# Kernel tuning notes

Measured on AMD Instinct MI355X. Metric: run time of the kernel, lower is better.

The kernel has to match this reference:

```python
import jax, jax.numpy as jnp
import numpy as np

IN_DIM = 256
HIDDEN = 64


def setup_inputs() -> dict:
    key = jax.random.key(0)
    k1, k2, k3, k4, k5, k6 = jax.random.split(key, 6)
    N, M, D, H = 2048, 2048, IN_DIM, HIDDEN
    # Kaiming-uniform-ish init scales (matching nn.Linear defaults loosely)
    lim1 = 1.0 / np.sqrt(2 * D)
    lim2 = 1.0 / np.sqrt(H)
    return {
        "ag_embed": jax.random.normal(k1, (N, D), dtype=jnp.float32),
        "ab_embed": jax.random.normal(k2, (M, D), dtype=jnp.float32),
        "W1": jax.random.uniform(k3, (2 * D, H), dtype=jnp.float32, minval=-lim1, maxval=lim1),
        "b1": jax.random.uniform(k4, (H,), dtype=jnp.float32, minval=-lim1, maxval=lim1),
        "W2": jax.random.uniform(k5, (H,), dtype=jnp.float32, minval=-lim2, maxval=lim2),
        "b2": jax.random.uniform(k6, (), dtype=jnp.float32, minval=-lim2, maxval=lim2),
    }


def reference(ag_embed, ab_embed, W1, b1, W2, b2):
    # Fused broadcast-concat + first linear:
    # cat([ag, ab]) @ W1 == ag @ W1[:D] + ab @ W1[D:]  (same math, no NxMx2D tensor)
    D = ag_embed.shape[1]
    ag_h = ag_embed @ W1[:D] + b1          # [N, H]
    ab_h = ab_embed @ W1[D:]               # [M, H]
    h = jax.nn.relu(ag_h[:, None, :] + ab_h[None, :, :])   # [N, M, H]
    logits = jnp.einsum("nmh,h->nm", h, W2) + b2            # [N, M]
    return jax.nn.sigmoid(logits)
```

## Files before the change

### kernel.cpp

```cpp
#include <hip/hip_runtime.h>
#include <hip/hip_bf16.h>

typedef float v2f __attribute__((ext_vector_type(2)));
typedef float v4f __attribute__((ext_vector_type(4)));

#define DD 256
#define HH 64

__global__ __launch_bounds__(256) void prep_kernel(
    const float* __restrict__ ag, const float* __restrict__ ab,
    const float* __restrict__ W1, const float* __restrict__ b1,
    float* __restrict__ U, float* __restrict__ V)
{
    __shared__ float a_tile[16 * DD];
    __shared__ float w_tile[DD * HH];

    const int t = threadIdx.x;
    const int b = blockIdx.x;
    const bool isV = (b >= 128);
    const float* __restrict__ A = isV ? ab : ag;
    const int row0 = (isV ? b - 128 : b) * 16;
    const float* __restrict__ W = W1 + (isV ? DD * HH : 0);

    {
        const v4f* As = (const v4f*)(A + row0 * DD);
        v4f* Ad = (v4f*)a_tile;
        #pragma unroll
        for (int i = 0; i < 4; ++i) Ad[t + i * 256] = As[t + i * 256];
        const v4f* Ws = (const v4f*)W;
        v4f* Wd = (v4f*)w_tile;
        #pragma unroll
        for (int i = 0; i < 16; ++i) Wd[t + i * 256] = Ws[t + i * 256];
    }
    __syncthreads();

    const int h = t & 63;
    const int g = t >> 6;
    float acc0 = 0.f, acc1 = 0.f, acc2 = 0.f, acc3 = 0.f;
    const float* __restrict__ ar = a_tile + (g * 4) * DD;
    #pragma unroll 8
    for (int k = 0; k < DD; ++k) {
        const float w = w_tile[k * HH + h];
        acc0 += ar[k]          * w;
        acc1 += ar[k + DD]     * w;
        acc2 += ar[k + 2 * DD] * w;
        acc3 += ar[k + 3 * DD] * w;
    }

    if (!isV) {
        const float bb = b1[h];
        float* Ur = U + (row0 + g * 4) * HH + h;
        Ur[0]      = acc0 + bb;
        Ur[HH]     = acc1 + bb;
        Ur[2 * HH] = acc2 + bb;
        Ur[3 * HH] = acc3 + bb;
    } else {
        __syncthreads();
        float* buf = a_tile;
        buf[(g * 4 + 0) * HH + h] = acc0;
        buf[(g * 4 + 1) * HH + h] = acc1;
        buf[(g * 4 + 2) * HH + h] = acc2;
        buf[(g * 4 + 3) * HH + h] = acc3;
        __syncthreads();
        const int hs = t >> 2, q = t & 3;
        v4f f;
        f.x = buf[(q * 4 + 0) * HH + hs];
        f.y = buf[(q * 4 + 1) * HH + hs];
        f.z = buf[(q * 4 + 2) * HH + hs];
        f.w = buf[(q * 4 + 3) * HH + hs];
        *(v4f*)(V + hs * 2048 + row0 + q * 4) = f;
    }
}

__global__ __launch_bounds__(256) void pair_kernel(
    const float* __restrict__ U, const float* __restrict__ V,
    const float* __restrict__ W2, const float* __restrict__ b2,
    float* __restrict__ out)
{
    __shared__ float u_lds[32 * HH];
    __shared__ float vt[HH * 128];
    __shared__ float w2_lds[HH];

    const int t = threadIdx.x;
    const int R = blockIdx.y * 32;
    const int C = blockIdx.x * 128;

    {
        const v4f* Us = (const v4f*)(U + R * HH);
        v4f* Ud = (v4f*)u_lds;
        Ud[t]       = Us[t];
        Ud[t + 256] = Us[t + 256];
        const float* Vb = V + C;
        v4f* Vd = (v4f*)vt;
        #pragma unroll
        for (int i = 0; i < 8; ++i) {
            const int flat = t + i * 256;
            const int hh = flat >> 5;
            const int cc = flat & 31;
            Vd[flat] = *(const v4f*)(Vb + hh * 2048 + cc * 4);
        }
        if (t < HH) w2_lds[t] = W2[t];
    }
    __syncthreads();

    const int lane = t & 63;
    const int wv = t >> 6;
    const int r0 = wv * 8;
    const int c0 = lane * 2;

    v2f acc[8];
    #pragma unroll
    for (int i = 0; i < 8; ++i) acc[i] = 0.0f;

    const v2f vzero = 0.0f;
    #pragma unroll 2
    for (int h0 = 0; h0 < HH; h0 += 4) {
        const v4f w4 = *(const v4f*)&w2_lds[h0];
        const v2f vf0 = *(const v2f*)&vt[(h0 + 0) * 128 + c0];
        const v2f vf1 = *(const v2f*)&vt[(h0 + 1) * 128 + c0];
        const v2f vf2 = *(const v2f*)&vt[(h0 + 2) * 128 + c0];
        const v2f vf3 = *(const v2f*)&vt[(h0 + 3) * 128 + c0];
        #pragma unroll
        for (int i = 0; i < 8; ++i) {
            const v4f uf = *(const v4f*)&u_lds[(r0 + i) * HH + h0];
            v2f t0 = vf0 + uf.x; t0 = __builtin_elementwise_max(t0, vzero); acc[i] += t0 * w4.x;
            v2f t1 = vf1 + uf.y; t1 = __builtin_elementwise_max(t1, vzero); acc[i] += t1 * w4.y;
            v2f t2 = vf2 + uf.z; t2 = __builtin_elementwise_max(t2, vzero); acc[i] += t2 * w4.z;
            v2f t3 = vf3 + uf.w; t3 = __builtin_elementwise_max(t3, vzero); acc[i] += t3 * w4.w;
        }
    }

    const float b2v = *b2;
    #pragma unroll
    for (int i = 0; i < 8; ++i) {
        const v2f x = acc[i] + b2v;
        float2 st;
        st.x = 1.0f / (1.0f + __expf(-x.x));
        st.y = 1.0f / (1.0f + __expf(-x.y));
        *(float2*)(out + (size_t)(R + r0 + i) * 2048 + C + c0) = st;
    }
}

extern "C" void kernel_launch(void* const* d_in, const int* in_sizes, int n_in,
                              void* d_out, int out_size, void* d_ws, size_t ws_size,
                              hipStream_t stream) {
    const float* ag = (const float*)d_in[0];
    const float* ab = (const float*)d_in[1];
    const float* W1 = (const float*)d_in[2];
    const float* b1 = (const float*)d_in[3];
    const float* W2 = (const float*)d_in[4];
    const float* b2 = (const float*)d_in[5];
    float* out = (float*)d_out;

    float* U = (float*)d_ws;
    float* V = U + 2048 * HH;

    prep_kernel<<<256, 256, 0, stream>>>(ag, ab, W1, b1, U, V);
    pair_kernel<<<dim3(16, 64), 256, 0, stream>>>(U, V, W2, b2, out);
}
```

Baseline: 97.95 us.

## Use packed fp16 with fdot2 in pair kernel and restructure prep kernel

The pairwise kernel now stores U and V as packed half2 and does the add, relu and W2 dot with packed fp16 math plus v_dot2 instructions, so each instruction handles twice as many elements. The column tile per block doubles and each thread produces four outputs. The prep kernel reads inputs straight from global memory instead of staging whole tiles in LDS, and writes fp16 outputs through a small padded buffer. Sigmoid uses a fast reciprocal. Half-precision intermediates lower accuracy and may exceed tolerance.

```diff
diff --git a/kernel.cpp b/kernel.cpp
--- a/kernel.cpp
+++ b/kernel.cpp
@@ -3,141 +3,179 @@
 
 typedef float v2f __attribute__((ext_vector_type(2)));
 typedef float v4f __attribute__((ext_vector_type(4)));
+typedef _Float16 h2v __attribute__((ext_vector_type(2)));
 
 #define DD 256
 #define HH 64
+#define H2 32
+
+#if __has_builtin(__builtin_amdgcn_fdot2)
+#define FDOT2(a, b, c) __builtin_amdgcn_fdot2((a), (b), (c), false)
+#else
+#define FDOT2(a, b, c) ((c) + (float)(a).x * (float)(b).x + (float)(a).y * (float)(b).y)
+#endif
+
+static __device__ __forceinline__ h2v as_h2(unsigned x) {
+    union { unsigned u; h2v h; } c; c.u = x; return c.h;
+}
+static __device__ __forceinline__ float fast_sigmoid(float x) {
+    return __builtin_amdgcn_rcpf(1.0f + __expf(-x));
+}
 
 __global__ __launch_bounds__(256) void prep_kernel(
     const float* __restrict__ ag, const float* __restrict__ ab,
     const float* __restrict__ W1, const float* __restrict__ b1,
-    float* __restrict__ U, float* __restrict__ V)
+    h2v* __restrict__ U, h2v* __restrict__ V)
 {
-    __shared__ float a_tile[16 * DD];
-    __shared__ float w_tile[DD * HH];
+    __shared__ float buf[16 * 66];
 
     const int t = threadIdx.x;
     const int b = blockIdx.x;
     const bool isV = (b >= 128);
     const float* __restrict__ A = isV ? ab : ag;
-    const int row0 = (isV ? b - 128 : b) * 16;
+    const int row0 = (b & 127) * 16;
     const float* __restrict__ W = W1 + (isV ? DD * HH : 0);
-
-    {
-        const v4f* As = (const v4f*)(A + row0 * DD);
-        v4f* Ad = (v4f*)a_tile;
-        #pragma unroll
-        for (int i = 0; i < 4; ++i) Ad[t + i * 256] = As[t + i * 256];
-        const v4f* Ws = (const v4f*)W;
-        v4f* Wd = (v4f*)w_tile;
-        #pragma unroll
-        for (int i = 0; i < 16; ++i) Wd[t + i * 256] = Ws[t + i * 256];
-    }
-    __syncthreads();
 
     const int h = t & 63;
     const int g = t >> 6;
+    const float* __restrict__ a0 = A + (row0 + g * 4) * DD;
+
     float acc0 = 0.f, acc1 = 0.f, acc2 = 0.f, acc3 = 0.f;
-    const float* __restrict__ ar = a_tile + (g * 4) * DD;
-    #pragma unroll 8
-    for (int k = 0; k < DD; ++k) {
-        const float w = w_tile[k * HH + h];
-        acc0 += ar[k]          * w;
-        acc1 += ar[k + DD]     * w;
-        acc2 += ar[k + 2 * DD] * w;
-        acc3 += ar[k + 3 * DD] * w;
+    #pragma unroll 2
+    for (int k = 0; k < DD; k += 4) {
+        const float w0 = W[(k + 0) * HH + h];
+        const float w1 = W[(k + 1) * HH + h];
+        const float w2_ = W[(k + 2) * HH + h];
+        const float w3 = W[(k + 3) * HH + h];
+        const v4f aa0 = *(const v4f*)(a0 + k);
+        const v4f aa1 = *(const v4f*)(a0 + DD + k);
+        const v4f aa2 = *(const v4f*)(a0 + 2 * DD + k);
+        const v4f aa3 = *(const v4f*)(a0 + 3 * DD + k);
+        acc0 = fmaf(aa0.x, w0, acc0); acc0 = fmaf(aa0.y, w1, acc0);
+        acc0 = fmaf(aa0.z, w2_, acc0); acc0 = fmaf(aa0.w, w3, acc0);
+        acc1 = fmaf(aa1.x, w0, acc1); acc1 = fmaf(aa1.y, w1, acc1);
+        acc1 = fmaf(aa1.z, w2_, acc1); acc1 = fmaf(aa1.w, w3, acc1);
+        acc2 = fmaf(aa2.x, w0, acc2); acc2 = fmaf(aa2.y, w1, acc2);
+        acc2 = fmaf(aa2.z, w2_, acc2); acc2 = fmaf(aa2.w, w3, acc2);
+        acc3 = fmaf(aa3.x, w0, acc3); acc3 = fmaf(aa3.y, w1, acc3);
+        acc3 = fmaf(aa3.z, w2_, acc3); acc3 = fmaf(aa3.w, w3, acc3);
     }
 
     if (!isV) {
         const float bb = b1[h];
-        float* Ur = U + (row0 + g * 4) * HH + h;
-        Ur[0]      = acc0 + bb;
-        Ur[HH]     = acc1 + bb;
-        Ur[2 * HH] = acc2 + bb;
-        Ur[3 * HH] = acc3 + bb;
-    } else {
-        __syncthreads();
-        float* buf = a_tile;
-        buf[(g * 4 + 0) * HH + h] = acc0;
-        buf[(g * 4 + 1) * HH + h] = acc1;
-        buf[(g * 4 + 2) * HH + h] = acc2;
-        buf[(g * 4 + 3) * HH + h] = acc3;
-        __syncthreads();
-        const int hs = t >> 2, q = t & 3;
-        v4f f;
-        f.x = buf[(q * 4 + 0) * HH + hs];
-        f.y = buf[(q * 4 + 1) * HH + hs];
-        f.z = buf[(q * 4 + 2) * HH + hs];
-        f.w = buf[(q * 4 + 3) * HH + hs];
-        *(v4f*)(V + hs * 2048 + row0 + q * 4) = f;
+        acc0 += bb; acc1 += bb; acc2 += bb; acc3 += bb;
+    }
+
+    buf[(g * 4 + 0) * 66 + h] = acc0;
+    buf[(g * 4 + 1) * 66 + h] = acc1;
+    buf[(g * 4 + 2) * 66 + h] = acc2;
+    buf[(g * 4 + 3) * 66 + h] = acc3;
+    __syncthreads();
+
+    #pragma unroll
+    for (int i = 0; i < 2; ++i) {
+        const int flat = t + i * 256;
+        if (!isV) {
+            const int r = flat >> 5, h2 = flat & 31;
+            h2v p;
+            p.x = (_Float16)buf[r * 66 + 2 * h2];
+            p.y = (_Float16)buf[r * 66 + 2 * h2 + 1];
+            U[(row0 + r) * H2 + h2] = p;
+        } else {
+            const int c = flat & 15, h2 = flat >> 4;
+            h2v p;
+            p.x = (_Float16)buf[c * 66 + 2 * h2];
+            p.y = (_Float16)buf[c * 66 + 2 * h2 + 1];
+            V[h2 * 2048 + row0 + c] = p;
+        }
     }
 }
 
-__global__ __launch_bounds__(256) void pair_kernel(
-    const float* __restrict__ U, const float* __restrict__ V,
+__global__ __launch_bounds__(256, 2) void pair_kernel(
+    const h2v* __restrict__ U, const h2v* __restrict__ V,
     const float* __restrict__ W2, const float* __restrict__ b2,
     float* __restrict__ out)
 {
-    __shared__ float u_lds[32 * HH];
-    __shared__ float vt[HH * 128];
-    __shared__ float w2_lds[HH];
+    __shared__ unsigned u_lds[32 * H2];
+    __shared__ unsigned vt[H2 * 256];
+    __shared__ h2v w2l[H2];
 
     const int t = threadIdx.x;
     const int R = blockIdx.y * 32;
-    const int C = blockIdx.x * 128;
+    const int C = blockIdx.x * 256;
 
     {
-        const v4f* Us = (const v4f*)(U + R * HH);
-        v4f* Ud = (v4f*)u_lds;
-        Ud[t]       = Us[t];
-        Ud[t + 256] = Us[t + 256];
-        const float* Vb = V + C;
-        v4f* Vd = (v4f*)vt;
+        const uint4* Us = (const uint4*)(U + R * H2);
+        ((uint4*)u_lds)[t] = Us[t];
+        const uint4* Vs = (const uint4*)V;
+        uint4* Vd = (uint4*)vt;
         #pragma unroll
         for (int i = 0; i < 8; ++i) {
             const int flat = t + i * 256;
-            const int hh = flat >> 5;
-            const int cc = flat & 31;
-            Vd[flat] = *(const v4f*)(Vb + hh * 2048 + cc * 4);
+            const int row = flat >> 6, c4 = flat & 63;
+            Vd[flat] = Vs[row * 512 + (C >> 2) + c4];
         }
-        if (t < HH) w2_lds[t] = W2[t];
+        if (t < H2) {
+            h2v p; p.x = (_Float16)W2[2 * t]; p.y = (_Float16)W2[2 * t + 1];
+            w2l[t] = p;
+        }
     }
     __syncthreads();
 
     const int lane = t & 63;
     const int wv = t >> 6;
     const int r0 = wv * 8;
-    const int c0 = lane * 2;
 
-    v2f acc[8];
+    float acc[8][4];
     #pragma unroll
-    for (int i = 0; i < 8; ++i) acc[i] = 0.0f;
+    for (int i = 0; i < 8; ++i)
+        #pragma unroll
+        for (int k = 0; k < 4; ++k) acc[i][k] = 0.0f;
 
-    const v2f vzero = 0.0f;
-    #pragma unroll 2
-    for (int h0 = 0; h0 < HH; h0 += 4) {
-        const v4f w4 = *(const v4f*)&w2_lds[h0];
-        const v2f vf0 = *(const v2f*)&vt[(h0 + 0) * 128 + c0];
-        const v2f vf1 = *(const v2f*)&vt[(h0 + 1) * 128 + c0];
-        const v2f vf2 = *(const v2f*)&vt[(h0 + 2) * 128 + c0];
-        const v2f vf3 = *(const v2f*)&vt[(h0 + 3) * 128 + c0];
+    const h2v zero = {(_Float16)0.0f, (_Float16)0.0f};
+    const uint4* ub = (const uint4*)u_lds;
+    const uint4* vb = (const uint4*)vt;
+
+    #pragma unroll
+    for (int hc = 0; hc < 8; ++hc) {
+        const uint4 wq = *((const uint4*)w2l + hc);
+        const h2v w0 = as_h2(wq.x), w1 = as_h2(wq.y), w2_ = as_h2(wq.z), w3 = as_h2(wq.w);
+
+        h2v vv[4][4];
+        #pragma unroll
+        for (int j = 0; j < 4; ++j) {
+            const uint4 q = vb[(hc * 4 + j) * 64 + lane];
+            vv[j][0] = as_h2(q.x); vv[j][1] = as_h2(q.y);
+            vv[j][2] = as_h2(q.z); vv[j][3] = as_h2(q.w);
+        }
+
         #pragma unroll
         for (int i = 0; i < 8; ++i) {
-            const v4f uf = *(const v4f*)&u_lds[(r0 + i) * HH + h0];
-            v2f t0 = vf0 + uf.x; t0 = __builtin_elementwise_max(t0, vzero); acc[i] += t0 * w4.x;
-            v2f t1 = vf1 + uf.y; t1 = __builtin_elementwise_max(t1, vzero); acc[i] += t1 * w4.y;
-            v2f t2 = vf2 + uf.z; t2 = __builtin_elementwise_max(t2, vzero); acc[i] += t2 * w4.z;
-            v2f t3 = vf3 + uf.w; t3 = __builtin_elementwise_max(t3, vzero); acc[i] += t3 * w4.w;
+            const uint4 uq = ub[(r0 + i) * 8 + hc];
+            const h2v u0 = as_h2(uq.x), u1 = as_h2(uq.y), u2 = as_h2(uq.z), u3 = as_h2(uq.w);
+            #pragma unroll
+            for (int k = 0; k < 4; ++k) {
+                h2v s0 = u0 + vv[0][k]; s0 = __builtin_elementwise_max(s0, zero);
+                acc[i][k] = FDOT2(s0, w0, acc[i][k]);
+                h2v s1 = u1 + vv[1][k]; s1 = __builtin_elementwise_max(s1, zero);
+                acc[i][k] = FDOT2(s1, w1, acc[i][k]);
+                h2v s2 = u2 + vv[2][k]; s2 = __builtin_elementwise_max(s2, zero);
+                acc[i][k] = FDOT2(s2, w2_, acc[i][k]);
+                h2v s3 = u3 + vv[3][k]; s3 = __builtin_elementwise_max(s3, zero);
+                acc[i][k] = FDOT2(s3, w3, acc[i][k]);
+            }
         }
     }
 
     const float b2v = *b2;
     #pragma unroll
     for (int i = 0; i < 8; ++i) {
-        const v2f x = acc[i] + b2v;
-        float2 st;
-        st.x = 1.0f / (1.0f + __expf(-x.x));
-        st.y = 1.0f / (1.0f + __expf(-x.y));
-        *(float2*)(out + (size_t)(R + r0 + i) * 2048 + C + c0) = st;
+        v4f o;
+        o.x = fast_sigmoid(acc[i][0] + b2v);
+        o.y = fast_sigmoid(acc[i][1] + b2v);
+        o.z = fast_sigmoid(acc[i][2] + b2v);
+        o.w = fast_sigmoid(acc[i][3] + b2v);
+        *(v4f*)(out + (size_t)(R + r0 + i) * 2048 + C + lane * 4) = o;
     }
 }
 
@@ -152,9 +190,9 @@
     const float* b2 = (const float*)d_in[5];
     float* out = (float*)d_out;
 
-    float* U = (float*)d_ws;
-    float* V = U + 2048 * HH;
+    h2v* U = (h2v*)d_ws;
+    h2v* V = U + 2048 * H2;
 
     prep_kernel<<<256, 256, 0, stream>>>(ag, ab, W1, b1, U, V);
-    pair_kernel<<<dim3(16, 64), 256, 0, stream>>>(U, V, W2, b2, out);
+    pair_kernel<<<dim3(8, 64), 256, 0, stream>>>(U, V, W2, b2, out);
 }
```

Measured after the change: 99.18 us. No clear change (+1.2%).
